# Performance work log

Measured on AMD Instinct MI355X. Metric: run time of the kernel, lower is better.

Reference implementation:

```python
import jax, jax.numpy as jnp
import numpy as np
from jax import lax

SEQ, B, F, L = 32, 32, 64, 256
OC = 128          # out_channels
K = 5
PAD = (K - 1) // 2
GROUPS = 4 * OC // 32  # GroupNorm groups = 16
EPS = 1e-5


def group_norm(x, w, b):
    # x: (B, C, L); normalize over each group's (C//G, L) slice
    bsz, c, l = x.shape
    xg = x.reshape(bsz, GROUPS, -1)
    mu = jnp.mean(xg, axis=-1, keepdims=True)
    var = jnp.var(xg, axis=-1, keepdims=True)
    xg = (xg - mu) * lax.rsqrt(var + EPS)
    return xg.reshape(bsz, c, l) * w[None, :, None] + b[None, :, None]


def setup_inputs() -> dict:
    key = jax.random.key(0)
    k1, k2, k3 = jax.random.split(key, 3)
    fan_in = (F + OC) * K
    return {
        "inputs": jax.random.normal(k1, (SEQ, B, F, L), dtype=jnp.float32),
        "conv_w": jax.random.normal(k2, (4 * OC, F + OC, K), dtype=jnp.float32) / np.sqrt(fan_in),
        "conv_b": jax.random.normal(k3, (4 * OC,), dtype=jnp.float32) * 0.01,
        "gn_w": jnp.ones((4 * OC,), dtype=jnp.float32),
        "gn_b": jnp.zeros((4 * OC,), dtype=jnp.float32),
    }


def reference(inputs, conv_w, conv_b, gn_w, gn_b):
    bsz, sub_len = inputs.shape[1], inputs.shape[3]
    hx0 = jnp.zeros((bsz, OC, sub_len), dtype=inputs.dtype)
    cx0 = jnp.zeros((bsz, OC, sub_len), dtype=inputs.dtype)

    def step(carry, x):
        hx, cx = carry
        combined = jnp.concatenate([x, hx], axis=1)  # (B, F+OC, L)
        gates = lax.conv_general_dilated(
            combined, conv_w, window_strides=(1,), padding=[(PAD, PAD)],
            dimension_numbers=("NCH", "OIH", "NCH"))
        gates = gates + conv_b[None, :, None]
        gates = group_norm(gates, gn_w, gn_b)
        i, f, g, o = jnp.split(gates, 4, axis=1)
        cy = jax.nn.sigmoid(f) * cx + jax.nn.sigmoid(i) * jnp.tanh(g)
        hy = jax.nn.sigmoid(o) * jnp.tanh(cy)
        return (hy, cy), hy

    (hy, cy), outputs = lax.scan(step, (hx0, cx0), inputs)
    return outputs, (hy, cy)
```

## Files before the change

kernel.cpp:

```cpp
#include <hip/hip_runtime.h>

typedef unsigned short u16;
typedef unsigned int u32;
typedef unsigned long long u64;
typedef __attribute__((ext_vector_type(4))) float f32x4;
typedef __attribute__((ext_vector_type(8))) short s16x8;
typedef __attribute__((ext_vector_type(4))) int i32x4;

#define EPS 1e-5f

__device__ __forceinline__ u16 f2bf(float f) {
  unsigned u = __float_as_uint(f);
  return (u16)((u + 0x7fffu + ((u >> 16) & 1u)) >> 16);
}
__device__ __forceinline__ float sigm(float x) { return 1.0f / (1.0f + __expf(-x)); }
__device__ __forceinline__ float tanh_f(float x) {
  float e = __expf(-2.0f * fabsf(x));
  float r = (1.0f - e) / (1.0f + e);
  return copysignf(r, x);
}
__device__ __forceinline__ void gl_lds16(const void* g, void* l) {
  __builtin_amdgcn_global_load_lds(
      (const __attribute__((address_space(1))) u32*)g,
      (__attribute__((address_space(3))) u32*)l, 16, 0, 0);
}

__global__ __launch_bounds__(256) void k_setup(
    const float* __restrict__ cw, u16* __restrict__ Wpk,
    const float* __restrict__ x, u16* __restrict__ xT,
    i32x4* __restrict__ hTz, i32x4* __restrict__ cxz, i32x4* __restrict__ flz) {
  const int bid = blockIdx.x, tid = threadIdx.x;
  __shared__ __align__(16) u16 ltile[256 * 72];
  if (bid < 1920) {
    int idx = bid * 256 + tid;
    int f = idx >> 9, r = idx & 511;
    int lane = r >> 3, j = r & 7;
    int of = f & 31, tk = f >> 5;
    int kk = tk % 6, tap = tk / 6;
    int o = (of << 4) + (lane & 15);
    int c = (kk << 5) + ((lane >> 4) << 3) + j;
    int g = of >> 3, cs = (of >> 1) & 3, wm = of & 1;
    int newpos = (cs << 3) + (wm << 2) + g;
    Wpk[(((tk << 5) + newpos) << 9) + r] = f2bf(cw[(o * 192 + c) * 5 + tap]);
  } else if (bid < 2944) {
    int tb = bid - 1920;
    const float* src = x + tb * (64 * 256);
    for (int it = 0; it < 64; ++it) {
      int idx = it * 256 + tid;
      int c = idx >> 8, l = idx & 255;
      ltile[l * 72 + c] = f2bf(src[idx]);
    }
    __syncthreads();
    char* dst = (char*)(xT + tb * 16896);
    i32x4 z = {0, 0, 0, 0};
    for (int i = tid; i < 2112; i += 256) {
      int r = i >> 3, ch = i & 7;
      i32x4 v = z;
      if (r >= 2 && r < 258) v = *(const i32x4*)(ltile + (r - 2) * 72 + ch * 8);
      *(i32x4*)(dst + r * 128 + ((ch * 16) ^ ((r & 7) << 4))) = v;
    }
  } else {
    int base = (bid - 2944) * 256 + tid;
    i32x4 z = {0, 0, 0, 0};
    for (int i = base; i < 270336; i += 131072) hTz[i] = z;
    for (int i = base; i < 262144; i += 131072) cxz[i] = z;
    for (int i = base; i < 2048;   i += 131072) flz[i] = z;
  }
}

__global__ __launch_bounds__(512) void k_step(
    const u16* __restrict__ Wpk, const u16* __restrict__ xT, u16* __restrict__ hT,
    const float* __restrict__ cb, const float* __restrict__ gnw, const float* __restrict__ gnb,
    float* __restrict__ cx, float* __restrict__ out,
    float* __restrict__ stats, int* __restrict__ flags, int t) {
  const int bid = blockIdx.x;
  const int b = bid & 31, lh = (bid >> 5) & 1, cs = bid >> 6;
  const int L0 = lh << 7;
  const int tid = threadIdx.x, wave = tid >> 6, lane = tid & 63;
  const int wm = wave & 1, wl = wave >> 1;
  const int l15 = lane & 15, q = lane >> 4;
  const int cgrp = q << 4;

  __shared__ __align__(16) char ldsx[16896];
  __shared__ __align__(16) char ldsh[33792];
  __shared__ __align__(16) char hl[8192];
  __shared__ float red[8][4][2];
  __shared__ float smu[4], srs[4];

  const u16* hTr = hT + (t & 1) * 1081344;
  u16* hTw = hT + ((t + 1) & 1) * 1081344;

  {
    const char* gx = (const char*)(xT + ((t << 5) + b) * 16896) + (lh << 14);
    for (int i = tid; i < 1056; i += 512) gl_lds16(gx + (i << 4), ldsx + (i << 4));
  }
  __builtin_amdgcn_sched_barrier(0);
  {
    const char* gh = (const char*)hTr + b * 67584 + (lh << 15);
    for (int i = tid; i < 2112; i += 512) gl_lds16(gh + (i << 4), ldsh + (i << 4));
  }
  __builtin_amdgcn_sched_barrier(0);
  asm volatile("s_waitcnt vmcnt(4)" ::: "memory");
  __builtin_amdgcn_s_barrier();
  __builtin_amdgcn_sched_barrier(0);

  f32x4 zero4 = {0.f, 0.f, 0.f, 0.f};
  f32x4 acc[4][2];
  #pragma unroll
  for (int g = 0; g < 4; ++g) { acc[g][0] = zero4; acc[g][1] = zero4; }

  const s16x8* Wv = (const s16x8*)Wpk;
  const int abase = (cs << 3) + (wm << 2);

  #pragma unroll
  for (int tap = 0; tap < 5; ++tap) {
    #pragma unroll
    for (int kk = 0; kk < 2; ++kk) {
      const int cc = tap * 6 + kk;
      const s16x8* Wb = Wv + (((cc << 5) + abase) << 6) + lane;
      s16x8 av[4], bv[2];
      #pragma unroll
      for (int g = 0; g < 4; ++g) av[g] = Wb[g << 6];
      #pragma unroll
      for (int ni = 0; ni < 2; ++ni) {
        const int rr = (wl << 5) + (ni << 4) + l15 + tap;
        const int sw = (rr & 7) << 4;
        bv[ni] = *(const s16x8*)(ldsx + (rr << 7) + (((kk << 6) + cgrp) ^ sw));
      }
      #pragma unroll
      for (int g = 0; g < 4; ++g) {
        acc[g][0] = __builtin_amdgcn_mfma_f32_16x16x32_bf16(av[g], bv[0], acc[g][0], 0, 0, 0);
        acc[g][1] = __builtin_amdgcn_mfma_f32_16x16x32_bf16(av[g], bv[1], acc[g][1], 0, 0, 0);
      }
    }
  }
  __builtin_amdgcn_sched_barrier(0);
  asm volatile("s_waitcnt vmcnt(0)" ::: "memory");
  __builtin_amdgcn_s_barrier();
  __builtin_amdgcn_sched_barrier(0);

  #pragma unroll
  for (int tap = 0; tap < 5; ++tap) {
    #pragma unroll
    for (int kk2 = 0; kk2 < 4; ++kk2) {
      const int cc = tap * 6 + kk2 + 2;
      const s16x8* Wb = Wv + (((cc << 5) + abase) << 6) + lane;
      s16x8 av[4], bv[2];
      #pragma unroll
      for (int g = 0; g < 4; ++g) av[g] = Wb[g << 6];
      #pragma unroll
      for (int ni = 0; ni < 2; ++ni) {
        const int rr = (wl << 5) + (ni << 4) + l15 + tap;
        const int sw = (rr & 7) << 4;
        bv[ni] = *(const s16x8*)(ldsh + (rr << 8) + (((kk2 << 6) + cgrp) ^ sw));
      }
      #pragma unroll
      for (int g = 0; g < 4; ++g) {
        acc[g][0] = __builtin_amdgcn_mfma_f32_16x16x32_bf16(av[g], bv[0], acc[g][0], 0, 0, 0);
        acc[g][1] = __builtin_amdgcn_mfma_f32_16x16x32_bf16(av[g], bv[1], acc[g][1], 0, 0, 0);
      }
    }
  }

  const int chq = (cs << 5) + (wm << 4) + (q << 2);
  float sum4[4], sq4[4];
  #pragma unroll
  for (int g = 0; g < 4; ++g) {
    const f32x4 bias = *(const f32x4*)(cb + (g << 7) + chq);
    sum4[g] = 0.f; sq4[g] = 0.f;
    #pragma unroll
    for (int ni = 0; ni < 2; ++ni)
      #pragma unroll
      for (int r = 0; r < 4; ++r) {
        float v = acc[g][ni][r] + bias[r];
        acc[g][ni][r] = v;
        sum4[g] += v; sq4[g] += v * v;
      }
  }
  f32x4 w4[4], b4[4];
  float cxv[2][4];
  #pragma unroll
  for (int g = 0; g < 4; ++g) {
    w4[g] = *(const f32x4*)(gnw + (g << 7) + chq);
    b4[g] = *(const f32x4*)(gnb + (g << 7) + chq);
  }
  #pragma unroll
  for (int ni = 0; ni < 2; ++ni) {
    const int l = L0 + (wl << 5) + (ni << 4) + l15;
    #pragma unroll
    for (int r = 0; r < 4; ++r)
      cxv[ni][r] = cx[(b << 15) + ((chq + r) << 8) + l];
  }
  #pragma unroll
  for (int off = 1; off < 64; off <<= 1) {
    #pragma unroll
    for (int g = 0; g < 4; ++g) {
      sum4[g] += __shfl_xor(sum4[g], off);
      sq4[g]  += __shfl_xor(sq4[g], off);
    }
  }
  if (lane == 0) {
    #pragma unroll
    for (int g = 0; g < 4; ++g) { red[wave][g][0] = sum4[g]; red[wave][g][1] = sq4[g]; }
  }
  __syncthreads();

  const int sidx = (((t << 5) + b) << 3) + (cs << 1) + lh;
  if (tid == 0) {
    float* sp = stats + (sidx << 3);
    #pragma unroll
    for (int g = 0; g < 4; ++g) {
      float s = 0.f, qv = 0.f;
      #pragma unroll
      for (int w = 0; w < 8; ++w) { s += red[w][g][0]; qv += red[w][g][1]; }
      __hip_atomic_store(sp + (g << 1),     s,  __ATOMIC_RELAXED, __HIP_MEMORY_SCOPE_AGENT);
      __hip_atomic_store(sp + (g << 1) + 1, qv, __ATOMIC_RELAXED, __HIP_MEMORY_SCOPE_AGENT);
    }
    __hip_atomic_store(&flags[sidx], 1, __ATOMIC_RELEASE, __HIP_MEMORY_SCOPE_AGENT);
    while (__hip_atomic_load(&flags[sidx ^ 1], __ATOMIC_RELAXED, __HIP_MEMORY_SCOPE_AGENT) == 0)
      __builtin_amdgcn_s_sleep(2);
    __builtin_amdgcn_fence(__ATOMIC_ACQUIRE, "agent");
    const float* pe = stats + ((sidx & ~1) << 3);
    const float* po = stats + ((sidx | 1) << 3);
    const float inv = 1.0f / 8192.0f;
    #pragma unroll
    for (int g = 0; g < 4; ++g) {
      float s = __hip_atomic_load(pe + (g << 1), __ATOMIC_RELAXED, __HIP_MEMORY_SCOPE_AGENT)
              + __hip_atomic_load(po + (g << 1), __ATOMIC_RELAXED, __HIP_MEMORY_SCOPE_AGENT);
      float qv = __hip_atomic_load(pe + (g << 1) + 1, __ATOMIC_RELAXED, __HIP_MEMORY_SCOPE_AGENT)
               + __hip_atomic_load(po + (g << 1) + 1, __ATOMIC_RELAXED, __HIP_MEMORY_SCOPE_AGENT);
      float m = s * inv;
      smu[g] = m;
      srs[g] = rsqrtf(qv * inv - m * m + EPS);
    }
  }
  __syncthreads();

  const float mu0 = smu[0], mu1 = smu[1], mu2 = smu[2], mu3 = smu[3];
  const float rs0 = srs[0], rs1 = srs[1], rs2 = srs[2], rs3 = srs[3];
  float* outp = out + (((t << 5) + b) << 15);
  #pragma unroll
  for (int ni = 0; ni < 2; ++ni) {
    const int l = L0 + (wl << 5) + (ni << 4) + l15;
    const int ll = l - L0;
    u16 hp[4];
    #pragma unroll
    for (int r = 0; r < 4; ++r) {
      const int c = chq + r;
      float vi = (acc[0][ni][r] - mu0) * rs0 * w4[0][r] + b4[0][r];
      float vf = (acc[1][ni][r] - mu1) * rs1 * w4[1][r] + b4[1][r];
      float vg = (acc[2][ni][r] - mu2) * rs2 * w4[2][r] + b4[2][r];
      float vo = (acc[3][ni][r] - mu3) * rs3 * w4[3][r] + b4[3][r];
      float cyv = sigm(vf) * cxv[ni][r] + sigm(vi) * tanh_f(vg);
      float hyv = sigm(vo) * tanh_f(cyv);
      const int ci = (c << 8) + l;
      cx[(b << 15) + ci] = cyv;
      outp[ci] = hyv;
      hp[r] = f2bf(hyv);
      if (t == 31) {
        out[33554432 + (b << 15) + ci] = hyv;
        out[34603008 + (b << 15) + ci] = cyv;
      }
    }
    *(u64*)(hl + (ll << 6) + (((wm << 5) + (q << 3)) ^ ((ll & 3) << 4))) =
        *(const u64*)hp;
  }
  __syncthreads();

  {
    const int ll = tid >> 2, k = tid & 3;
    const int row = L0 + ll + 2;
    i32x4 v = *(const i32x4*)(hl + (ll << 6) + ((k << 4) ^ ((ll & 3) << 4)));
    char* dst = (char*)hTw + b * 67584 + (row << 8) +
                ((((cs << 2) + k) << 4) ^ ((row & 7) << 4));
    *(i32x4*)dst = v;
  }
}

extern "C" void kernel_launch(void* const* d_in, const int* in_sizes, int n_in,
                              void* d_out, int out_size, void* d_ws, size_t ws_size,
                              hipStream_t stream) {
  const float* x  = (const float*)d_in[0];
  const float* cw = (const float*)d_in[1];
  const float* cb = (const float*)d_in[2];
  const float* gw = (const float*)d_in[3];
  const float* gb = (const float*)d_in[4];
  float* out = (float*)d_out;
  char* ws = (char*)d_ws;

  u16*   Wpk   = (u16*)(ws);
  u16*   xT    = (u16*)(ws + 983040);
  u16*   hT    = (u16*)(ws + 35586048);
  float* cx    = (float*)(ws + 39911424);
  float* stats = (float*)(ws + 44105728);
  int*   flags = (int*)(ws + 44367872);

  k_setup<<<3456, 256, 0, stream>>>(cw, Wpk, x, xT, (i32x4*)hT, (i32x4*)cx, (i32x4*)flags);
  for (int t = 0; t < 32; ++t)
    k_step<<<256, 512, 0, stream>>>(Wpk, xT, hT, cb, gw, gb, cx, out, stats, flags, t);
}
```

Measured before the change: 686.7 us.

## Repartition step blocks to full sequence length with 16-channel slices

Each block previously covered half the sequence length and 32 channels across two M-waves. It now covers the full length of 256 with a single 16-channel group per block, using 8 waves along L. The whole x and h tiles are loaded into LDS, which doubles LDS use to about 110KB and forces one block per CU. The goal is to remove the duplicated halo loads across L halves and to change how weights are reused, at the cost of more LDS traffic per block and lower occupancy.

Measured after the change: 704.2 us. +2.6%, slower.

```diff
diff --git a/kernel.cpp b/kernel.cpp
--- a/kernel.cpp
+++ b/kernel.cpp
@@ -68,21 +68,20 @@
   }
 }
 
-__global__ __launch_bounds__(512) void k_step(
+__global__ __launch_bounds__(512, 1) void k_step(
     const u16* __restrict__ Wpk, const u16* __restrict__ xT, u16* __restrict__ hT,
     const float* __restrict__ cb, const float* __restrict__ gnw, const float* __restrict__ gnb,
     float* __restrict__ cx, float* __restrict__ out,
     float* __restrict__ stats, int* __restrict__ flags, int t) {
   const int bid = blockIdx.x;
-  const int b = bid & 31, lh = (bid >> 5) & 1, cs = bid >> 6;
-  const int L0 = lh << 7;
+  const int b = bid & 31, ch16 = bid >> 5;
   const int tid = threadIdx.x, wave = tid >> 6, lane = tid & 63;
-  const int wm = wave & 1, wl = wave >> 1;
+  const int wl = wave;
   const int l15 = lane & 15, q = lane >> 4;
   const int cgrp = q << 4;
 
-  __shared__ __align__(16) char ldsx[16896];
-  __shared__ __align__(16) char ldsh[33792];
+  __shared__ __align__(16) char ldsx[33792];
+  __shared__ __align__(16) char ldsh[67584];
   __shared__ __align__(16) char hl[8192];
   __shared__ float red[8][4][2];
   __shared__ float smu[4], srs[4];
@@ -91,16 +90,16 @@
   u16* hTw = hT + ((t + 1) & 1) * 1081344;
 
   {
-    const char* gx = (const char*)(xT + ((t << 5) + b) * 16896) + (lh << 14);
-    for (int i = tid; i < 1056; i += 512) gl_lds16(gx + (i << 4), ldsx + (i << 4));
+    const char* gx = (const char*)(xT + ((t << 5) + b) * 16896);
+    for (int i = tid; i < 2112; i += 512) gl_lds16(gx + (i << 4), ldsx + (i << 4));
   }
   __builtin_amdgcn_sched_barrier(0);
   {
-    const char* gh = (const char*)hTr + b * 67584 + (lh << 15);
-    for (int i = tid; i < 2112; i += 512) gl_lds16(gh + (i << 4), ldsh + (i << 4));
-  }
-  __builtin_amdgcn_sched_barrier(0);
-  asm volatile("s_waitcnt vmcnt(4)" ::: "memory");
+    const char* gh = (const char*)hTr + b * 67584;
+    for (int i = tid; i < 4224; i += 512) gl_lds16(gh + (i << 4), ldsh + (i << 4));
+  }
+  __builtin_amdgcn_sched_barrier(0);
+  asm volatile("s_waitcnt vmcnt(8)" ::: "memory");
   __builtin_amdgcn_s_barrier();
   __builtin_amdgcn_sched_barrier(0);
 
@@ -110,7 +109,7 @@
   for (int g = 0; g < 4; ++g) { acc[g][0] = zero4; acc[g][1] = zero4; }
 
   const s16x8* Wv = (const s16x8*)Wpk;
-  const int abase = (cs << 3) + (wm << 2);
+  const int abase = ((ch16 >> 1) << 3) + ((ch16 & 1) << 2);
 
   #pragma unroll
   for (int tap = 0; tap < 5; ++tap) {
@@ -162,7 +161,7 @@
     }
   }
 
-  const int chq = (cs << 5) + (wm << 4) + (q << 2);
+  const int chq = (ch16 << 4) + (q << 2);
   float sum4[4], sq4[4];
   #pragma unroll
   for (int g = 0; g < 4; ++g) {
@@ -186,7 +185,7 @@
   }
   #pragma unroll
   for (int ni = 0; ni < 2; ++ni) {
-    const int l = L0 + (wl << 5) + (ni << 4) + l15;
+    const int l = (wl << 5) + (ni << 4) + l15;
     #pragma unroll
     for (int r = 0; r < 4; ++r)
       cxv[ni][r] = cx[(b << 15) + ((chq + r) << 8) + l];
@@ -205,7 +204,7 @@
   }
   __syncthreads();
 
-  const int sidx = (((t << 5) + b) << 3) + (cs << 1) + lh;
+  const int sidx = (((t << 5) + b) << 3) + ch16;
   if (tid == 0) {
     float* sp = stats + (sidx << 3);
     #pragma unroll
@@ -241,8 +240,7 @@
   float* outp = out + (((t << 5) + b) << 15);
   #pragma unroll
   for (int ni = 0; ni < 2; ++ni) {
-    const int l = L0 + (wl << 5) + (ni << 4) + l15;
-    const int ll = l - L0;
+    const int l = (wl << 5) + (ni << 4) + l15;
     u16 hp[4];
     #pragma unroll
     for (int r = 0; r < 4; ++r) {
@@ -262,17 +260,16 @@
         out[34603008 + (b << 15) + ci] = cyv;
       }
     }
-    *(u64*)(hl + (ll << 6) + (((wm << 5) + (q << 3)) ^ ((ll & 3) << 4))) =
-        *(const u64*)hp;
+    *(u64*)(hl + (l << 5) + ((q << 3) ^ ((l & 1) << 4))) = *(const u64*)hp;
   }
   __syncthreads();
 
   {
-    const int ll = tid >> 2, k = tid & 3;
-    const int row = L0 + ll + 2;
-    i32x4 v = *(const i32x4*)(hl + (ll << 6) + ((k << 4) ^ ((ll & 3) << 4)));
-    char* dst = (char*)hTw + b * 67584 + (row << 8) +
-                ((((cs << 2) + k) << 4) ^ ((row & 7) << 4));
+    const int l = tid >> 1, k = tid & 1;
+    const int row = l + 2;
+    i32x4 v = *(const i32x4*)(hl + (l << 5) + ((k << 4) ^ ((l & 1) << 4)));
+    const int gk = (ch16 << 1) + k;
+    char* dst = (char*)hTw + b * 67584 + (row << 8) + ((gk << 4) ^ ((row & 7) << 4));
     *(i32x4*)dst = v;
   }
 }
```
